# Kernel optimization log

Hardware: AMD Instinct MI355X
Metric: run time of the kernel (lower is better)

The kernel has to match this reference:

```python
import jax, jax.numpy as jnp
import numpy as np

B, S, D = 2, 2048, 1024
H, HD = 16, 64          # num_heads, head_dim = D // H
W = 31                  # window_size (odd)
E = 1024                # embed_dim


def setup_inputs() -> dict:
    key = jax.random.key(0)
    ks = jax.random.split(key, 12)
    sd = 1.0 / np.sqrt(D)
    so = 1.0 / np.sqrt(H * HD)
    return {
        "x": jax.random.normal(ks[0], (B, S, D), jnp.float32),
        "fsq": jax.random.normal(ks[1], (1, S, D), jnp.float32),   # feature_squeeze_token
        "pos": jax.random.normal(ks[2], (1, S, D), jnp.float32),   # position_token
        "Wq": jax.random.normal(ks[3], (H, D, HD), jnp.float32) * sd,
        "bq": jax.random.normal(ks[4], (H, HD), jnp.float32) * sd,
        "Wk": jax.random.normal(ks[5], (H, D, HD), jnp.float32) * sd,
        "bk": jax.random.normal(ks[6], (H, HD), jnp.float32) * sd,
        "Wv": jax.random.normal(ks[7], (H, D, HD), jnp.float32) * sd,
        "bv": jax.random.normal(ks[8], (H, HD), jnp.float32) * sd,
        "Wo": jax.random.normal(ks[9], (H * HD, E), jnp.float32) * so,
        "bo": jax.random.normal(ks[10], (E,), jnp.float32) * so,
    }


def reference(x, fsq, pos, Wq, bq, Wk, bk, Wv, bv, Wo, bo):
    b, s, d = x.shape
    pad = (W - 1) // 2
    # sliding windows: (B, S, W, D), zero-padded at sequence edges
    xp = jnp.pad(x, ((0, 0), (pad, pad), (0, 0)))
    idx = jnp.arange(s)[:, None] + jnp.arange(W)[None, :]  # (S, W)
    win = xp[:, idx, :]  # (B, S, W, D)
    a = jnp.broadcast_to(fsq[:, :, None, :], (b, s, 1, d))  # squeeze token per pos
    bt = jnp.broadcast_to(pos[:, :, None, :], (b, s, 1, d))  # position token per pos
    kv = jnp.concatenate([win, bt, a], axis=2)  # (B, S, K=W+2, D)
    q = jnp.broadcast_to(fsq, (b, s, d))        # query = squeeze token
    # per-head projections (heads stacked on axis h)
    qh = jnp.einsum("bsd,hde->bhse", q, Wq) + bq[None, :, None, :]        # (B,H,S,HD)
    kh = jnp.einsum("bskd,hde->bhske", kv, Wk) + bk[None, :, None, None, :]
    vh = jnp.einsum("bskd,hde->bhske", kv, Wv) + bv[None, :, None, None, :]
    scores = jnp.einsum("bhse,bhske->bhsk", qh, kh) / jnp.sqrt(jnp.asarray(HD, x.dtype))
    attn = jax.nn.softmax(scores, axis=-1)  # dropout is identity in eval
    outh = jnp.einsum("bhsk,bhske->bhse", attn, vh)  # (B,H,S,HD)
    concat = outh.transpose(0, 2, 1, 3).reshape(b, s, H * HD)  # heads concat order 0..H-1
    return concat @ Wo + bo  # (B, S, E)
```

## Files before the change

### kernel.cpp

```cpp
#include <hip/hip_runtime.h>


typedef __attribute__((ext_vector_type(8))) short bf16x8;
typedef __attribute__((ext_vector_type(4))) float f32x4;
typedef unsigned short u16;
typedef unsigned int u32;
typedef unsigned long long u64;

__device__ __forceinline__ float bf2f(u16 u) {
  union { u32 i; float f; } v; v.i = ((u32)u) << 16; return v.f;
}
__device__ __forceinline__ u16 f2bf(float f) {
  union { float f; u32 i; } v; v.f = f;
  u32 r = v.i + 0x7fffu + ((v.i >> 16) & 1u);
  return (u16)(r >> 16);
}
__device__ __forceinline__ float2 unpk(u32 u) {
  union { u32 i; float f; } lo, hi;
  lo.i = u << 16; hi.i = u & 0xffff0000u;
  return make_float2(lo.f, hi.f);
}
__device__ __forceinline__ float dot8(uint4 a, uint4 b) {
  float s = 0.f;
  { float2 x = unpk(a.x), y = unpk(b.x); s += x.x*y.x + x.y*y.y; }
  { float2 x = unpk(a.y), y = unpk(b.y); s += x.x*y.x + x.y*y.y; }
  { float2 x = unpk(a.z), y = unpk(b.z); s += x.x*y.x + x.y*y.y; }
  { float2 x = unpk(a.w), y = unpk(b.w); s += x.x*y.x + x.y*y.y; }
  return s;
}
__device__ __forceinline__ void gload_lds16(const u16* g, u16* l) {
  __builtin_amdgcn_global_load_lds((const __attribute__((address_space(1))) void*)(g),
                                   (__attribute__((address_space(3))) void*)(l),
                                   16, 0, 0);
}
__device__ __forceinline__ uint4 pack8(float4 a, float4 b) {
  union { u16 h[8]; uint4 q; } u;
  u.h[0] = f2bf(a.x); u.h[1] = f2bf(a.y); u.h[2] = f2bf(a.z); u.h[3] = f2bf(a.w);
  u.h[4] = f2bf(b.x); u.h[5] = f2bf(b.y); u.h[6] = f2bf(b.z); u.h[7] = f2bf(b.w);
  return u.q;
}

__device__ __forceinline__ void transpose_body(const float* src, u16* dst,
                                               int R, int C, int r0, int c0) {
  __shared__ u16 tile[64][72];
  int t = threadIdx.x;
#pragma unroll
  for (int i = 0; i < 16; ++i) {
    int idx = i * 256 + t;
    int r = idx >> 6, c = idx & 63;
    tile[r][c] = f2bf(src[(size_t)(r0 + r) * C + (c0 + c)]);
  }
  __syncthreads();
#pragma unroll
  for (int i = 0; i < 16; ++i) {
    int idx = i * 256 + t;
    int c = idx >> 6, r = idx & 63;
    dst[(size_t)(c0 + c) * R + (r0 + r)] = tile[r][c];
  }
}

__global__ __launch_bounds__(256) void prep(const float* __restrict__ x,
                                            const float* __restrict__ fsq,
                                            const float* __restrict__ pos,
                                            const float* __restrict__ Wq,
                                            const float* __restrict__ Wk,
                                            const float* __restrict__ Wv,
                                            const float* __restrict__ Wo,
                                            u16* __restrict__ xb,
                                            u16* __restrict__ fsqb,
                                            u16* __restrict__ posb,
                                            u16* __restrict__ WqT,
                                            u16* __restrict__ WkT,
                                            u16* __restrict__ WvT,
                                            u16* __restrict__ WoT) {
  int bid = blockIdx.x;
  if (bid < 4096) {
    int i = bid * 256 + threadIdx.x;
    const float* src; u16* dst; int off;
    if (i < 524288)      { src = x;   dst = xb;   off = i; }
    else if (i < 786432) { src = fsq; dst = fsqb; off = i - 524288; }
    else                 { src = pos; dst = posb; off = i - 786432; }
    float4 a = ((const float4*)src)[2 * off];
    float4 b = ((const float4*)src)[2 * off + 1];
    ((uint4*)dst)[off] = pack8(a, b);
  } else {
    int id = bid - 4096;
    int z = id >> 8, rest = id & 255;
    int xx = rest & 15, yy = rest >> 4;
    if (z < 3) {
      const float* s = (z == 0) ? Wq : (z == 1) ? Wk : Wv;
      u16* d = (z == 0) ? WqT : (z == 1) ? WkT : WvT;
      size_t off = (size_t)xx * 65536;
      transpose_body(s + off, d + off, 1024, 64, yy * 64, 0);
    } else {
      transpose_body(Wo, WoT, 1024, 1024, yy * 64, xx * 64);
    }
  }
}

__device__ __forceinline__ int swz(int R, int c) {
  return (R * 8 + (c ^ (R & 7))) * 8;
}

__global__ __launch_bounds__(256) void proj_gemm(const u16* __restrict__ xb,
                                                 const u16* __restrict__ fsqb,
                                                 const u16* __restrict__ posb,
                                                 const u16* __restrict__ WkT,
                                                 const u16* __restrict__ WvT,
                                                 const u16* __restrict__ WqT,
                                                 const float* __restrict__ bk,
                                                 const float* __restrict__ bv,
                                                 const float* __restrict__ bq,
                                                 u16* __restrict__ Kp,
                                                 u16* __restrict__ VpT,
                                                 u16* __restrict__ Vd,
                                                 u16* __restrict__ Qp) {
  __shared__ u16 As[128 * 64];
  __shared__ u16 Bs[128 * 64];

  const int bid = blockIdx.x;
  const int lb = (bid & 7) * 144 + (bid >> 3);
  const int t = threadIdx.x, lane = t & 63, wave = t >> 6;
  const int row16 = lane & 15, quad = lane >> 4;
  const int l8 = lane >> 3;
  const int cswz = (lane & 7) ^ l8;

  const u16 *Ap, *BT;
  const float* bias;
  u16* Crm = nullptr;
  u16* Cvt = nullptr;
  int noff = 0, tmb = 0;

  if (lb < 1024) {
    int tm = lb >> 4, tn = lb & 15;
    if (tm < 32)      Ap = xb   + (size_t)tm * 131072;
    else if (tm < 48) Ap = fsqb + (size_t)(tm - 32) * 131072;
    else              Ap = posb + (size_t)(tm - 48) * 131072;
    if (tn < 8) {
      BT = WkT + (size_t)(tn * 128) * 1024;
      bias = bk;
      Crm = Kp + (size_t)tm * 131072;
      noff = tn * 128;
    } else {
      BT = WvT + (size_t)((tn - 8) * 128) * 1024;
      bias = bv;
      noff = (tn - 8) * 128;
      if (tm < 32) { Cvt = VpT; tmb = tm * 128; }
      else         { Crm = Vd + (size_t)(tm - 32) * 131072; }
    }
  } else {
    int q2 = lb - 1024;
    int tm = q2 >> 3, tn = q2 & 7;
    Ap = fsqb + (size_t)tm * 131072;
    BT = WqT + (size_t)(tn * 128) * 1024;
    bias = bq;
    Crm = Qp + (size_t)tm * 131072;
    noff = tn * 128;
  }

  const int wm = (wave >> 1) * 64, wn = (wave & 1) * 64;
  f32x4 acc[4][4] = {};

  for (int k0 = 0; k0 < 1024; k0 += 64) {
    __syncthreads();
#pragma unroll
    for (int j = 0; j < 4; ++j) {
      int r = wave * 32 + j * 8 + l8;
      gload_lds16(Ap + (size_t)r * 1024 + k0 + cswz * 8,
                  &As[wave * 2048 + j * 512]);
    }
#pragma unroll
    for (int j = 0; j < 4; ++j) {
      int r = wave * 32 + j * 8 + l8;
      gload_lds16(BT + (size_t)r * 1024 + k0 + cswz * 8,
                  &Bs[wave * 2048 + j * 512]);
    }
    __syncthreads();

#pragma unroll
    for (int kb = 0; kb < 2; ++kb) {
      bf16x8 a_frag[4], b_frag[4];
#pragma unroll
      for (int i = 0; i < 4; ++i)
        a_frag[i] = *(const bf16x8*)&As[swz(wm + i * 16 + row16, kb * 4 + quad)];
#pragma unroll
      for (int j = 0; j < 4; ++j)
        b_frag[j] = *(const bf16x8*)&Bs[swz(wn + j * 16 + row16, kb * 4 + quad)];
#pragma unroll
      for (int i = 0; i < 4; ++i)
#pragma unroll
        for (int j = 0; j < 4; ++j)
          acc[i][j] = __builtin_amdgcn_mfma_f32_16x16x32_bf16(
              a_frag[i], b_frag[j], acc[i][j], 0, 0, 0);
    }
  }

  if (Cvt) {
#pragma unroll
    for (int j = 0; j < 4; ++j) {
      int nv = noff + wn + j * 16 + row16;
      float bb = bias[nv];
#pragma unroll
      for (int i = 0; i < 4; ++i) {
        int m0 = wm + i * 16 + quad * 4;
        union { u16 h[4]; u64 q; } o;
#pragma unroll
        for (int r = 0; r < 4; ++r) o.h[r] = f2bf(acc[i][j][r] + bb);
        *(u64*)(Cvt + (size_t)nv * 4096 + tmb + m0) = o.q;
      }
    }
  } else {
#pragma unroll
    for (int j = 0; j < 4; ++j) {
      int n = noff + wn + j * 16 + row16;
      float bb = bias[n];
#pragma unroll
      for (int i = 0; i < 4; ++i) {
        int m0 = wm + i * 16 + quad * 4;
#pragma unroll
        for (int r = 0; r < 4; ++r)
          Crm[(size_t)(m0 + r) * 1024 + n] = f2bf(acc[i][j][r] + bb);
      }
    }
  }
}

__global__ __launch_bounds__(256) void out_gemm(const u16* __restrict__ Att,
                                                const u16* __restrict__ WoT,
                                                const float* __restrict__ bo,
                                                float* __restrict__ Out) {
  __shared__ u16 As[64 * 128];
  __shared__ u16 Bs[128 * 128];
  const int bid = blockIdx.x;
  const int lb = (bid & 7) * 64 + (bid >> 3);
  const int tile_n = (lb & 7) * 128;
  const int tm = lb >> 3;
  const u16* Ap = Att + (size_t)tm * 65536;
  float* Cp = Out + (size_t)tm * 65536;

  const int t = threadIdx.x, lane = t & 63, wave = t >> 6;
  const int wm = (wave >> 1) * 32, wn = (wave & 1) * 64;
  const int row16 = lane & 15, quad = lane >> 4;

  f32x4 acc[2][4] = {};

  for (int k0 = 0; k0 < 1024; k0 += 128) {
    __syncthreads();
#pragma unroll
    for (int j = 0; j < 4; ++j) {
      int idx = wave * 256 + j * 64 + lane;
      int r = idx >> 4, c = (idx & 15) ^ (r & 15);
      gload_lds16(Ap + (size_t)r * 1024 + k0 + c * 8,
                  &As[wave * 2048 + j * 512]);
    }
#pragma unroll
    for (int j = 0; j < 8; ++j) {
      int idx = wave * 512 + j * 64 + lane;
      int r = idx >> 4, c = (idx & 15) ^ (r & 15);
      gload_lds16(WoT + (size_t)(tile_n + r) * 1024 + k0 + c * 8,
                  &Bs[wave * 4096 + j * 512]);
    }
    __syncthreads();

#pragma unroll
    for (int kb = 0; kb < 4; ++kb) {
      bf16x8 a_frag[2], b_frag[4];
#pragma unroll
      for (int i = 0; i < 2; ++i) {
        int R = wm + i * 16 + row16, c = kb * 4 + quad;
        a_frag[i] = *(const bf16x8*)&As[(R * 16 + (c ^ (R & 15))) * 8];
      }
#pragma unroll
      for (int j = 0; j < 4; ++j) {
        int R = wn + j * 16 + row16, c = kb * 4 + quad;
        b_frag[j] = *(const bf16x8*)&Bs[(R * 16 + (c ^ (R & 15))) * 8];
      }
#pragma unroll
      for (int i = 0; i < 2; ++i)
#pragma unroll
        for (int j = 0; j < 4; ++j)
          acc[i][j] = __builtin_amdgcn_mfma_f32_16x16x32_bf16(
              a_frag[i], b_frag[j], acc[i][j], 0, 0, 0);
    }
  }

#pragma unroll
  for (int j = 0; j < 4; ++j) {
    int n = tile_n + wn + j * 16 + row16;
    float bb = bo[n];
#pragma unroll
    for (int i = 0; i < 2; ++i) {
      int m0 = wm + i * 16 + quad * 4;
#pragma unroll
      for (int r = 0; r < 4; ++r)
        Cp[(size_t)(m0 + r) * 1024 + n] = acc[i][j][r] + bb;
    }
  }
}

#define QS   0
#define KPS  2304
#define KFS  4608
#define KWS  6912
#define VTS  11008
#define SMT  15104

__global__ __launch_bounds__(256) void attn_tile(const u16* __restrict__ Qp,
                                                 const u16* __restrict__ Kp,
                                                 const u16* __restrict__ VpT,
                                                 const u16* __restrict__ Vd,
                                                 const float* __restrict__ bk,
                                                 const float* __restrict__ bv,
                                                 u16* __restrict__ Att) {
  __shared__ u16 sm[SMT];
  __shared__ float smP[32 * 36];

  const int t = threadIdx.x;
  const int bid = blockIdx.x;
  const int s0 = (bid & 63) * 32;
  const int h  = (bid >> 6) & 15;
  const int b  = bid >> 10;
  const int lane = t & 63, wave = t >> 6;
  const int row16 = lane & 15, quad = lane >> 4;
  const int hcol = h * 64;

  { int w = t >> 3, oct = t & 7;
    *(uint4*)&sm[QS + w * 72 + oct * 8] =
        *(const uint4*)(Qp + (size_t)(s0 + w) * 1024 + hcol + oct * 8); }
  { int r = t >> 3, oct = t & 7;
    *(uint4*)&sm[KPS + r * 72 + oct * 8] =
        *(const uint4*)(Kp + (size_t)(6144 + s0 + r) * 1024 + hcol + oct * 8);
    *(uint4*)&sm[KFS + r * 72 + oct * 8] =
        *(const uint4*)(Kp + (size_t)(4096 + s0 + r) * 1024 + hcol + oct * 8); }

  const bool boundary = (s0 == 0) || (s0 == 2016);
  if (!boundary) {
#pragma unroll
    for (int i = 0; i < 2; ++i) {
      int task = i * 256 + t;
      int w = task >> 3, oct = task & 7;
      gload_lds16(Kp + (size_t)(b * 2048 + s0 + w - 16) * 1024 + hcol + oct * 8,
                  &sm[KWS + (i * 256 + wave * 64) * 8]);
      int e = w;
      gload_lds16(VpT + (size_t)(hcol + e) * 4096 + (b * 2048 + s0 - 16) + oct * 8,
                  &sm[VTS + (i * 256 + wave * 64) * 8]);
    }
  } else {
#pragma unroll
    for (int i = 0; i < 2; ++i) {
      int task = i * 256 + t;
      int w = task >> 3, oct = task & 7;
      int g = s0 + w - 16;
      uint4 kv;
      if ((unsigned)g < 2048u)
        kv = *(const uint4*)(Kp + (size_t)(b * 2048 + g) * 1024 + hcol + oct * 8);
      else
        kv = pack8(*(const float4*)(bk + hcol + oct * 8),
                   *(const float4*)(bk + hcol + oct * 8 + 4));
      *(uint4*)&sm[KWS + w * 64 + oct * 8] = kv;

      int e = w;
      int g0 = s0 + oct * 8 - 16;
      uint4 vv;
      if (g0 >= 0 && g0 + 7 < 2048)
        vv = *(const uint4*)(VpT + (size_t)(hcol + e) * 4096 + (b * 2048 + g0));
      else {
        u16 hb = f2bf(bv[hcol + e]);
        u32 pp = (u32)hb | ((u32)hb << 16);
        vv = make_uint4(pp, pp, pp, pp);
      }
      *(uint4*)&sm[VTS + e * 64 + oct * 8] = vv;
    }
  }
  __syncthreads();

  {
    f32x4 accS[2] = {};
#pragma unroll
    for (int kc = 0; kc < 2; ++kc) {
      bf16x8 bf_ = *(const bf16x8*)&sm[KWS + (wave * 16 + row16) * 64 + kc * 32 + quad * 8];
#pragma unroll
      for (int mi = 0; mi < 2; ++mi) {
        bf16x8 af = *(const bf16x8*)&sm[QS + (mi * 16 + row16) * 72 + kc * 32 + quad * 8];
        accS[mi] = __builtin_amdgcn_mfma_f32_16x16x32_bf16(af, bf_, accS[mi], 0, 0, 0);
      }
    }
#pragma unroll
    for (int mi = 0; mi < 2; ++mi)
#pragma unroll
      for (int r = 0; r < 4; ++r) {
        int s = mi * 16 + quad * 4 + r;
        int w = wave * 16 + row16;
        int d = w - s;
        if (d >= 1 && d <= 31) smP[s * 36 + d - 1] = accS[mi][r] * 0.125f;
      }
  }
  if (t < 64) {
    int s = t >> 1, which = t & 1;
    int base = (which == 0) ? KPS : KFS;
    float a = 0.f;
#pragma unroll
    for (int c = 0; c < 8; ++c)
      a += dot8(*(const uint4*)&sm[QS + s * 72 + c * 8],
                *(const uint4*)&sm[base + s * 72 + c * 8]);
    smP[s * 36 + 31 + which] = a * 0.125f;
  }
  __syncthreads();

  if (t < 64) {
    const int s = t >> 1, half = t & 1;
    const int kb_ = half * 17;
    float vals[17];
#pragma unroll
    for (int k = 0; k < 17; ++k) {
      int kk = kb_ + k;
      vals[k] = (kk < 33) ? smP[s * 36 + kk] : -1e30f;
    }
    float mx = -1e30f;
#pragma unroll
    for (int k = 0; k < 17; ++k) mx = fmaxf(mx, vals[k]);
    mx = fmaxf(mx, __shfl_xor(mx, 1, 64));
    float sum = 0.f;
#pragma unroll
    for (int k = 0; k < 17; ++k) { vals[k] = __expf(vals[k] - mx); sum += vals[k]; }
    sum += __shfl_xor(sum, 1, 64);
    const float inv = 1.f / sum;
    u32* prow = (u32*)&sm[QS + s * 72];
#pragma unroll
    for (int j = 0; j < 16; ++j) prow[half * 16 + j] = 0;
#pragma unroll
    for (int k = 0; k < 17; ++k) {
      int kk = kb_ + k;
      if (kk < 31)      sm[QS + s * 72 + (s + 1 + kk)] = f2bf(vals[k] * inv);
      else if (kk < 33) smP[s * 36 + 2 + kk] = vals[k] * inv;
    }
  }
  __syncthreads();

  {
    f32x4 accO[2] = {};
#pragma unroll
    for (int kc = 0; kc < 2; ++kc) {
      bf16x8 bf_ = *(const bf16x8*)&sm[VTS + (wave * 16 + row16) * 64 + kc * 32 + quad * 8];
#pragma unroll
      for (int mi = 0; mi < 2; ++mi) {
        bf16x8 af = *(const bf16x8*)&sm[QS + (mi * 16 + row16) * 72 + kc * 32 + quad * 8];
        accO[mi] = __builtin_amdgcn_mfma_f32_16x16x32_bf16(af, bf_, accO[mi], 0, 0, 0);
      }
    }
#pragma unroll
    for (int mi = 0; mi < 2; ++mi)
#pragma unroll
      for (int r = 0; r < 4; ++r) {
        int s = mi * 16 + quad * 4 + r;
        int e = wave * 16 + row16;
        float o = accO[mi][r]
                + smP[s * 36 + 33] * bf2f(Vd[(size_t)(2048 + s0 + s) * 1024 + hcol + e])
                + smP[s * 36 + 34] * bf2f(Vd[(size_t)(s0 + s) * 1024 + hcol + e]);
        Att[(size_t)(b * 2048 + s0 + s) * 1024 + hcol + e] = f2bf(o);
      }
  }
}

extern "C" void kernel_launch(void* const* d_in, const int* in_sizes, int n_in,
                              void* d_out, int out_size, void* d_ws, size_t ws_size,
                              hipStream_t stream) {
  (void)in_sizes; (void)n_in; (void)out_size; (void)ws_size;

  const float* x   = (const float*)d_in[0];
  const float* fsq = (const float*)d_in[1];
  const float* pos = (const float*)d_in[2];
  const float* Wq  = (const float*)d_in[3];
  const float* bq  = (const float*)d_in[4];
  const float* Wk  = (const float*)d_in[5];
  const float* bk  = (const float*)d_in[6];
  const float* Wv  = (const float*)d_in[7];
  const float* bv  = (const float*)d_in[8];
  const float* Wo  = (const float*)d_in[9];
  const float* bo  = (const float*)d_in[10];

  u16* ws = (u16*)d_ws;
  const size_t M1 = 1024 * 1024;
  u16* WqT  = ws + 0 * M1;
  u16* WkT  = ws + 1 * M1;
  u16* WvT  = ws + 2 * M1;
  u16* WoT  = ws + 3 * M1;
  u16* Qp   = ws + 4 * M1;
  u16* Kp   = ws + 6 * M1;
  u16* VpT  = ws + 14 * M1;
  u16* Vd   = ws + 18 * M1;
  u16* fsqb = ws + 22 * M1;
  u16* posb = ws + 24 * M1;
  u16* xb   = ws + 26 * M1;
  u16* Att  = ws + 22 * M1;

  prep<<<5120, 256, 0, stream>>>(x, fsq, pos, Wq, Wk, Wv, Wo,
                                 xb, fsqb, posb, WqT, WkT, WvT, WoT);

  proj_gemm<<<1152, 256, 0, stream>>>(xb, fsqb, posb, WkT, WvT, WqT,
                                      bk, bv, bq, Kp, VpT, Vd, Qp);

  attn_tile<<<2048, 256, 0, stream>>>(Qp, Kp, VpT, Vd, bk, bv, Att);

  out_gemm<<<512, 256, 0, stream>>>(Att, WoT, bo, (float*)d_out);
}
```

Baseline: 200.5 us.

## Rewrite projection GEMM as 256x256 tiles with 8 waves and pipelined LDS stages

The projection GEMM moves from 128x128 tiles with 4 waves to 256x256 tiles with 8 waves and 512 threads. A four-slot LDS ring prefetches the next A and B k-slices while MFMAs run. Fine-grained barriers, setprio and explicit vmcnt waits interleave loads with compute. The aim is more data reuse per tile and hidden global-load latency, at the cost of fewer blocks (288 on a 256-CU device), more LDS per block and higher register pressure.

Result: slower. 214.2 us (+6.8%).

```diff
diff --git a/kernel.cpp b/kernel.cpp
--- a/kernel.cpp
+++ b/kernel.cpp
@@ -98,11 +98,7 @@
   }
 }
 
-__device__ __forceinline__ int swz(int R, int c) {
-  return (R * 8 + (c ^ (R & 7))) * 8;
-}
-
-__global__ __launch_bounds__(256) void proj_gemm(const u16* __restrict__ xb,
+__global__ __launch_bounds__(512) void proj_gemm(const u16* __restrict__ xb,
                                                  const u16* __restrict__ fsqb,
                                                  const u16* __restrict__ posb,
                                                  const u16* __restrict__ WkT,
@@ -115,15 +111,15 @@
                                                  u16* __restrict__ VpT,
                                                  u16* __restrict__ Vd,
                                                  u16* __restrict__ Qp) {
-  __shared__ u16 As[128 * 64];
-  __shared__ u16 Bs[128 * 64];
+  __shared__ u16 AS[4][8192];
+  __shared__ u16 BS[4][8192];
 
   const int bid = blockIdx.x;
-  const int lb = (bid & 7) * 144 + (bid >> 3);
-  const int t = threadIdx.x, lane = t & 63, wave = t >> 6;
+  const int lb = (bid & 7) * 36 + (bid >> 3);
+  const int tid = threadIdx.x, lane = tid & 63, wave = tid >> 6;
   const int row16 = lane & 15, quad = lane >> 4;
-  const int l8 = lane >> 3;
-  const int cswz = (lane & 7) ^ l8;
+  const int wr = wave >> 2, wc = wave & 3;
+  const int bhalf = wc >> 1, bloc = (wc & 1) * 64;
 
   const u16 *Ap, *BT;
   const float* bias;
@@ -131,95 +127,184 @@
   u16* Cvt = nullptr;
   int noff = 0, tmb = 0;
 
-  if (lb < 1024) {
-    int tm = lb >> 4, tn = lb & 15;
-    if (tm < 32)      Ap = xb   + (size_t)tm * 131072;
-    else if (tm < 48) Ap = fsqb + (size_t)(tm - 32) * 131072;
-    else              Ap = posb + (size_t)(tm - 48) * 131072;
-    if (tn < 8) {
-      BT = WkT + (size_t)(tn * 128) * 1024;
+  if (lb < 256) {
+    int tm = lb >> 3, tn = lb & 7;
+    if (tm < 16)      Ap = xb   + (size_t)tm * 262144;
+    else if (tm < 24) Ap = fsqb + (size_t)(tm - 16) * 262144;
+    else              Ap = posb + (size_t)(tm - 24) * 262144;
+    if (tn < 4) {
+      BT = WkT + (size_t)(tn * 256) * 1024;
       bias = bk;
-      Crm = Kp + (size_t)tm * 131072;
-      noff = tn * 128;
+      Crm = Kp + (size_t)tm * 262144;
+      noff = tn * 256;
     } else {
-      BT = WvT + (size_t)((tn - 8) * 128) * 1024;
+      BT = WvT + (size_t)((tn - 4) * 256) * 1024;
       bias = bv;
-      noff = (tn - 8) * 128;
-      if (tm < 32) { Cvt = VpT; tmb = tm * 128; }
-      else         { Crm = Vd + (size_t)(tm - 32) * 131072; }
+      noff = (tn - 4) * 256;
+      if (tm < 16) { Cvt = VpT; tmb = tm * 256; }
+      else         { Crm = Vd + (size_t)(tm - 16) * 262144; }
     }
   } else {
-    int q2 = lb - 1024;
-    int tm = q2 >> 3, tn = q2 & 7;
-    Ap = fsqb + (size_t)tm * 131072;
-    BT = WqT + (size_t)(tn * 128) * 1024;
+    int q = lb - 256;
+    int tm = q >> 2, tn = q & 3;
+    Ap = fsqb + (size_t)tm * 262144;
+    BT = WqT + (size_t)(tn * 256) * 1024;
     bias = bq;
-    Crm = Qp + (size_t)tm * 131072;
-    noff = tn * 128;
-  }
-
-  const int wm = (wave >> 1) * 64, wn = (wave & 1) * 64;
-  f32x4 acc[4][4] = {};
-
-  for (int k0 = 0; k0 < 1024; k0 += 64) {
-    __syncthreads();
-#pragma unroll
-    for (int j = 0; j < 4; ++j) {
-      int r = wave * 32 + j * 8 + l8;
-      gload_lds16(Ap + (size_t)r * 1024 + k0 + cswz * 8,
-                  &As[wave * 2048 + j * 512]);
-    }
-#pragma unroll
-    for (int j = 0; j < 4; ++j) {
-      int r = wave * 32 + j * 8 + l8;
-      gload_lds16(BT + (size_t)r * 1024 + k0 + cswz * 8,
-                  &Bs[wave * 2048 + j * 512]);
-    }
-    __syncthreads();
-
-#pragma unroll
-    for (int kb = 0; kb < 2; ++kb) {
-      bf16x8 a_frag[4], b_frag[4];
-#pragma unroll
-      for (int i = 0; i < 4; ++i)
-        a_frag[i] = *(const bf16x8*)&As[swz(wm + i * 16 + row16, kb * 4 + quad)];
-#pragma unroll
-      for (int j = 0; j < 4; ++j)
-        b_frag[j] = *(const bf16x8*)&Bs[swz(wn + j * 16 + row16, kb * 4 + quad)];
-#pragma unroll
-      for (int i = 0; i < 4; ++i)
-#pragma unroll
-        for (int j = 0; j < 4; ++j)
-          acc[i][j] = __builtin_amdgcn_mfma_f32_16x16x32_bf16(
-              a_frag[i], b_frag[j], acc[i][j], 0, 0, 0);
-    }
+    Crm = Qp + (size_t)tm * 262144;
+    noff = tn * 256;
+  }
+
+  auto stage_half = [&](const u16* src, u16* dst) {
+#pragma unroll
+    for (int j = 0; j < 2; ++j) {
+      int slot = j * 512 + wave * 64 + lane;
+      int r = slot >> 3, cp = slot & 7;
+      gload_lds16(src + (size_t)r * 1024 + ((cp ^ (r & 7)) << 3),
+                  dst + ((j * 512 + wave * 64) << 3));
+    }
+  };
+  auto frag = [&](const u16* slot, int R, int c) -> bf16x8 {
+    return *(const bf16x8*)&slot[(R * 8 + (c ^ (R & 7))) * 8];
+  };
+
+  f32x4 acc[8][4] = {};
+
+  stage_half(Ap,                AS[0]);
+  stage_half(Ap + 131072,       AS[1]);
+  stage_half(BT,                BS[0]);
+  stage_half(BT + 131072,       BS[1]);
+  stage_half(Ap + 64,           AS[2]);
+  stage_half(Ap + 131072 + 64,  AS[3]);
+  asm volatile("s_waitcnt vmcnt(4)" ::: "memory");
+  __builtin_amdgcn_sched_barrier(0);
+  __builtin_amdgcn_s_barrier();
+
+  for (int kt = 0; kt < 16; ++kt) {
+    const u16* As_ = AS[(2 * kt + wr) & 3];
+    const u16* Bs_ = BS[(2 * kt + bhalf) & 3];
+    const bool stB = (kt + 1 < 16);
+    const bool stA = (kt + 2 < 16);
+
+    bf16x8 a_lo[4][2], a_hi[4][2], bf0[2][2], bf1[2][2];
+
+#pragma unroll
+    for (int i = 0; i < 4; ++i)
+#pragma unroll
+      for (int ks = 0; ks < 2; ++ks)
+        a_lo[i][ks] = frag(As_, i * 16 + row16, ks * 4 + quad);
+#pragma unroll
+    for (int j2 = 0; j2 < 2; ++j2)
+#pragma unroll
+      for (int ks = 0; ks < 2; ++ks)
+        bf0[j2][ks] = frag(Bs_, bloc + j2 * 16 + row16, ks * 4 + quad);
+    if (stB) stage_half(BT + (size_t)(kt + 1) * 64, BS[(2 * kt + 2) & 3]);
+    __builtin_amdgcn_s_barrier();
+    __builtin_amdgcn_s_setprio(1);
+#pragma unroll
+    for (int i = 0; i < 4; ++i)
+#pragma unroll
+      for (int j2 = 0; j2 < 2; ++j2)
+#pragma unroll
+        for (int ks = 0; ks < 2; ++ks)
+          acc[i][j2] = __builtin_amdgcn_mfma_f32_16x16x32_bf16(
+              a_lo[i][ks], bf0[j2][ks], acc[i][j2], 0, 0, 0);
+    __builtin_amdgcn_s_setprio(0);
+    __builtin_amdgcn_s_barrier();
+
+#pragma unroll
+    for (int i = 0; i < 4; ++i)
+#pragma unroll
+      for (int ks = 0; ks < 2; ++ks)
+        a_hi[i][ks] = frag(As_, 64 + i * 16 + row16, ks * 4 + quad);
+#pragma unroll
+    for (int j2 = 0; j2 < 2; ++j2)
+#pragma unroll
+      for (int ks = 0; ks < 2; ++ks)
+        bf1[j2][ks] = frag(Bs_, bloc + (j2 + 2) * 16 + row16, ks * 4 + quad);
+    if (stB) stage_half(BT + 131072 + (size_t)(kt + 1) * 64, BS[(2 * kt + 3) & 3]);
+    __builtin_amdgcn_s_barrier();
+    __builtin_amdgcn_s_setprio(1);
+#pragma unroll
+    for (int i = 0; i < 4; ++i)
+#pragma unroll
+      for (int j2 = 0; j2 < 2; ++j2)
+#pragma unroll
+        for (int ks = 0; ks < 2; ++ks)
+          acc[i][j2 + 2] = __builtin_amdgcn_mfma_f32_16x16x32_bf16(
+              a_lo[i][ks], bf1[j2][ks], acc[i][j2 + 2], 0, 0, 0);
+    __builtin_amdgcn_s_setprio(0);
+    __builtin_amdgcn_s_barrier();
+
+#pragma unroll
+    for (int j2 = 0; j2 < 2; ++j2)
+#pragma unroll
+      for (int ks = 0; ks < 2; ++ks)
+        bf0[j2][ks] = frag(Bs_, bloc + j2 * 16 + row16, ks * 4 + quad);
+    if (stA) stage_half(Ap + (size_t)(kt + 2) * 64, AS[(2 * kt) & 3]);
+    __builtin_amdgcn_s_barrier();
+    __builtin_amdgcn_s_setprio(1);
+#pragma unroll
+    for (int i = 0; i < 4; ++i)
+#pragma unroll
+      for (int j2 = 0; j2 < 2; ++j2)
+#pragma unroll
+        for (int ks = 0; ks < 2; ++ks)
+          acc[i + 4][j2] = __builtin_amdgcn_mfma_f32_16x16x32_bf16(
+              a_hi[i][ks], bf0[j2][ks], acc[i + 4][j2], 0, 0, 0);
+    __builtin_amdgcn_s_setprio(0);
+    __builtin_amdgcn_s_barrier();
+
+#pragma unroll
+    for (int j2 = 0; j2 < 2; ++j2)
+#pragma unroll
+      for (int ks = 0; ks < 2; ++ks)
+        bf1[j2][ks] = frag(Bs_, bloc + (j2 + 2) * 16 + row16, ks * 4 + quad);
+    if (stA) stage_half(Ap + 131072 + (size_t)(kt + 2) * 64, AS[(2 * kt + 1) & 3]);
+    if (kt <= 13) {
+      asm volatile("s_waitcnt vmcnt(4)" ::: "memory");
+    } else if (kt == 14) {
+      asm volatile("s_waitcnt vmcnt(0)" ::: "memory");
+    }
+    __builtin_amdgcn_sched_barrier(0);
+    __builtin_amdgcn_s_barrier();
+    __builtin_amdgcn_s_setprio(1);
+#pragma unroll
+    for (int i = 0; i < 4; ++i)
+#pragma unroll
+      for (int j2 = 0; j2 < 2; ++j2)
+#pragma unroll
+        for (int ks = 0; ks < 2; ++ks)
+          acc[i + 4][j2 + 2] = __builtin_amdgcn_mfma_f32_16x16x32_bf16(
+              a_hi[i][ks], bf1[j2][ks], acc[i + 4][j2 + 2], 0, 0, 0);
+    __builtin_amdgcn_s_setprio(0);
+    __builtin_amdgcn_s_barrier();
   }
 
   if (Cvt) {
 #pragma unroll
-    for (int j = 0; j < 4; ++j) {
-      int nv = noff + wn + j * 16 + row16;
+    for (int j2 = 0; j2 < 4; ++j2) {
+      int nv = noff + wc * 64 + j2 * 16 + row16;
       float bb = bias[nv];
 #pragma unroll
-      for (int i = 0; i < 4; ++i) {
-        int m0 = wm + i * 16 + quad * 4;
+      for (int i = 0; i < 8; ++i) {
+        int m0 = wr * 128 + i * 16 + quad * 4;
         union { u16 h[4]; u64 q; } o;
 #pragma unroll
-        for (int r = 0; r < 4; ++r) o.h[r] = f2bf(acc[i][j][r] + bb);
+        for (int r = 0; r < 4; ++r) o.h[r] = f2bf(acc[i][j2][r] + bb);
         *(u64*)(Cvt + (size_t)nv * 4096 + tmb + m0) = o.q;
       }
     }
   } else {
 #pragma unroll
-    for (int j = 0; j < 4; ++j) {
-      int n = noff + wn + j * 16 + row16;
+    for (int j2 = 0; j2 < 4; ++j2) {
+      int n = noff + wc * 64 + j2 * 16 + row16;
       float bb = bias[n];
 #pragma unroll
-      for (int i = 0; i < 4; ++i) {
-        int m0 = wm + i * 16 + quad * 4;
+      for (int i = 0; i < 8; ++i) {
+        int m0 = wr * 128 + i * 16 + quad * 4;
 #pragma unroll
         for (int r = 0; r < 4; ++r)
-          Crm[(size_t)(m0 + r) * 1024 + n] = f2bf(acc[i][j][r] + bb);
+          Crm[(size_t)(m0 + r) * 1024 + n] = f2bf(acc[i][j2][r] + bb);
       }
     }
   }
@@ -497,8 +582,8 @@
   prep<<<5120, 256, 0, stream>>>(x, fsq, pos, Wq, Wk, Wv, Wo,
                                  xb, fsqb, posb, WqT, WkT, WvT, WoT);
 
-  proj_gemm<<<1152, 256, 0, stream>>>(xb, fsqb, posb, WkT, WvT, WqT,
-                                      bk, bv, bq, Kp, VpT, Vd, Qp);
+  proj_gemm<<<288, 512, 0, stream>>>(xb, fsqb, posb, WkT, WvT, WqT,
+                                     bk, bv, bq, Kp, VpT, Vd, Qp);
 
   attn_tile<<<2048, 256, 0, stream>>>(Qp, Kp, VpT, Vd, bk, bv, Att);
 
```
